# Optimization experiments

Measured on AMD Instinct MI355X. Metric: run time of the kernel, lower is better.

## Reference

```python
import jax, jax.numpy as jnp
import numpy as np


def gcn_conv(x, edge_index, edge_weight, W, b):
    """PyG-style GCNConv: add self-loops, symmetric normalization, sum aggregation."""
    N = x.shape[0]
    h = x @ W  # [N, out]
    src, dst = edge_index[0], edge_index[1]
    loop = jnp.arange(N, dtype=src.dtype)
    src2 = jnp.concatenate([src, loop])
    dst2 = jnp.concatenate([dst, loop])
    w2 = jnp.concatenate([edge_weight, jnp.ones((N,), dtype=edge_weight.dtype)])
    deg = jax.ops.segment_sum(w2, dst2, num_segments=N)  # [N]
    dinv = jnp.where(deg > 0, jax.lax.rsqrt(jnp.where(deg > 0, deg, 1.0)), 0.0)
    norm = dinv[src2] * w2 * dinv[dst2]  # [E+N]
    msg = h[src2] * norm[:, None]  # [E+N, out]
    out = jax.ops.segment_sum(msg, dst2, num_segments=N)  # [N, out]
    return out + b


def setup_inputs() -> dict:
    key = jax.random.key(0)
    ks = jax.random.split(key, 10)
    N, E, F = 100000, 3200000, 128
    x = jax.random.normal(ks[0], (N, F), dtype=jnp.float32)
    edge_index = jax.random.randint(ks[1], (2, E), 0, N, dtype=jnp.int64)
    edge_weight = jax.random.uniform(ks[2], (E,), dtype=jnp.float32)
    s1 = 1.0 / np.sqrt(F)
    W1 = jax.random.uniform(ks[3], (F, 32), jnp.float32, -s1, s1)
    b1 = jnp.zeros((32,), jnp.float32)
    s2 = 1.0 / np.sqrt(32)
    W2 = jax.random.uniform(ks[4], (32, 16), jnp.float32, -s2, s2)
    b2 = jnp.zeros((16,), jnp.float32)
    s3 = 1.0 / np.sqrt(16)
    Wout = jax.random.uniform(ks[5], (16, 3), jnp.float32, -s3, s3)
    bout = jax.random.uniform(ks[6], (3,), jnp.float32, -s3, s3)
    return {"x": x, "edge_index": edge_index, "edge_weight": edge_weight,
            "W1": W1, "b1": b1, "W2": W2, "b2": b2, "Wout": Wout, "bout": bout}


def reference(x, edge_index, edge_weight, W1, b1, W2, b2, Wout, bout):
    h = jax.nn.relu(gcn_conv(x, edge_index, edge_weight, W1, b1))
    h = jax.nn.relu(gcn_conv(h, edge_index, edge_weight, W2, b2))
    return h @ Wout + bout  # [N, 3]
```

## Files before the change

kernel.cpp:

```cpp
#include <hip/hip_runtime.h>


#define BLK 256

__global__ void deg_kernel(const int* __restrict__ dst,
                           const float* __restrict__ w,
                           float* __restrict__ deg, int E) {
    int e = blockIdx.x * blockDim.x + threadIdx.x;
    if (e < E) atomicAdd(&deg[dst[e]], w[e]);
}

__global__ void dinv_kernel(float* __restrict__ deg, int N) {
    int i = blockIdx.x * blockDim.x + threadIdx.x;
    if (i < N) deg[i] = rsqrtf(deg[i] + 1.0f);
}

__global__ void gemm1_kernel(const float* __restrict__ x,
                             const float* __restrict__ W1,
                             const float* __restrict__ dinv,
                             float* __restrict__ g1, int N) {
    __shared__ float sW[128 * 32];
    __shared__ float sx[8][128];
    for (int i = threadIdx.x; i < 128 * 32; i += BLK) sW[i] = W1[i];
    int node0 = blockIdx.x * 8;
    for (int i = threadIdx.x; i < 8 * 128; i += BLK) {
        int r = i >> 7, c = i & 127;
        int n = node0 + r;
        sx[r][c] = (n < N) ? x[(long long)n * 128 + c] : 0.f;
    }
    __syncthreads();
    int local = threadIdx.x >> 5;
    int j = threadIdx.x & 31;
    int n = node0 + local;
    if (n < N) {
        float acc = 0.f;
#pragma unroll 16
        for (int k = 0; k < 128; k++) acc += sx[local][k] * sW[k * 32 + j];
        g1[n * 32 + j] = acc * dinv[n];
    }
}

template <int F>
__global__ void edge_agg_kernel(const int* __restrict__ src,
                                const int* __restrict__ dst,
                                const float* __restrict__ w,
                                const float* __restrict__ g,
                                float* __restrict__ agg, int E) {
    unsigned idx = blockIdx.x * blockDim.x + threadIdx.x;
    unsigned total = (unsigned)E * F;
    if (idx >= total) return;
    unsigned e = idx / F;
    unsigned f = idx & (F - 1);
    int s = __ldg(&src[e]);
    int d = __ldg(&dst[e]);
    float we = __ldg(&w[e]);
    atomicAdd(&agg[(unsigned)d * F + f], we * g[(unsigned)s * F + f]);
}

__global__ void layer2_kernel(const float* __restrict__ agg1,
                              const float* __restrict__ g1,
                              const float* __restrict__ dinv,
                              const float* __restrict__ b1,
                              const float* __restrict__ W2,
                              float* __restrict__ g2, int N) {
    __shared__ float sW[32 * 16];
    __shared__ float sin_[16][32];
    for (int i = threadIdx.x; i < 32 * 16; i += BLK) sW[i] = W2[i];
    int node0 = blockIdx.x * 16;
    for (int i = threadIdx.x; i < 16 * 32; i += BLK) {
        int r = i >> 5, c = i & 31;
        int n = node0 + r;
        float v = 0.f;
        if (n < N) {
            float di = dinv[n];
            v = fmaxf(di * (agg1[n * 32 + c] + g1[n * 32 + c]) + b1[c], 0.f);
        }
        sin_[r][c] = v;
    }
    __syncthreads();
    int local = threadIdx.x >> 4;
    int j = threadIdx.x & 15;
    int n = node0 + local;
    if (n < N) {
        float acc = 0.f;
#pragma unroll
        for (int k = 0; k < 32; k++) acc += sin_[local][k] * sW[k * 16 + j];
        g2[n * 16 + j] = acc * dinv[n];
    }
}

__global__ void final_kernel(const float* __restrict__ agg2,
                             const float* __restrict__ g2,
                             const float* __restrict__ dinv,
                             const float* __restrict__ b2,
                             const float* __restrict__ Wout,
                             const float* __restrict__ bout,
                             float* __restrict__ out, int N) {
    int n = blockIdx.x * blockDim.x + threadIdx.x;
    if (n >= N) return;
    float di = dinv[n];
    float o0 = bout[0], o1 = bout[1], o2 = bout[2];
#pragma unroll
    for (int k = 0; k < 16; k++) {
        float v = fmaxf(di * (agg2[n * 16 + k] + g2[n * 16 + k]) + b2[k], 0.f);
        o0 += v * Wout[k * 3 + 0];
        o1 += v * Wout[k * 3 + 1];
        o2 += v * Wout[k * 3 + 2];
    }
    out[n * 3 + 0] = o0;
    out[n * 3 + 1] = o1;
    out[n * 3 + 2] = o2;
}

extern "C" void kernel_launch(void* const* d_in, const int* in_sizes, int n_in,
                              void* d_out, int out_size, void* d_ws, size_t ws_size,
                              hipStream_t stream) {
    const float* x   = (const float*)d_in[0];
    const int* ei    = (const int*)d_in[1];
    const float* ew  = (const float*)d_in[2];
    const float* W1  = (const float*)d_in[3];
    const float* b1  = (const float*)d_in[4];
    const float* W2  = (const float*)d_in[5];
    const float* b2  = (const float*)d_in[6];
    const float* Wout = (const float*)d_in[7];
    const float* bout = (const float*)d_in[8];
    float* out = (float*)d_out;

    const int N = in_sizes[0] / 128;
    const int E = in_sizes[2];
    const int* src = ei;
    const int* dst = ei + E;

    float* ws   = (float*)d_ws;
    float* deg  = ws;
    float* agg1 = ws + (size_t)N;
    float* agg2 = ws + (size_t)33 * N;
    float* g1   = ws + (size_t)49 * N;
    float* g2   = ws + (size_t)81 * N;

    hipMemsetAsync(ws, 0, (size_t)49 * N * sizeof(float), stream);

    deg_kernel<<<(E + BLK - 1) / BLK, BLK, 0, stream>>>(dst, ew, deg, E);
    dinv_kernel<<<(N + BLK - 1) / BLK, BLK, 0, stream>>>(deg, N);

    gemm1_kernel<<<(N + 7) / 8, BLK, 0, stream>>>(x, W1, deg, g1, N);

    {
        unsigned total = (unsigned)E * 32u;
        edge_agg_kernel<32><<<(total + BLK - 1) / BLK, BLK, 0, stream>>>(
            src, dst, ew, g1, agg1, E);
    }

    layer2_kernel<<<(N + 15) / 16, BLK, 0, stream>>>(agg1, g1, deg, b1, W2, g2, N);

    {
        unsigned total = (unsigned)E * 16u;
        edge_agg_kernel<16><<<(total + BLK - 1) / BLK, BLK, 0, stream>>>(
            src, dst, ew, g2, agg2, E);
    }

    final_kernel<<<(N + BLK - 1) / BLK, BLK, 0, stream>>>(
        agg2, g2, deg, b2, Wout, bout, out, N);
}
```

Baseline: 836.0 us.

## Build CSR by destination and replace atomic push aggregation with pull

Counts in-degrees, prefix-scans them into row pointers and scatters (src, weight) pairs into a destination-sorted CSR array on every call. Aggregation then becomes a per-node, per-feature pull loop with no float atomics, and bias plus ReLU are fused into that loop. This removes the per-feature atomic traffic of the old edge kernels. In exchange it adds the CSR construction cost (an extra atomic histogram and a scatter with atomics over all edges), and the pull loop is imbalanced across nodes of different degree.

```diff
diff --git a/kernel.cpp b/kernel.cpp
--- a/kernel.cpp
+++ b/kernel.cpp
@@ -3,17 +3,81 @@
 
 #define BLK 256
 
-__global__ void deg_kernel(const int* __restrict__ dst,
-                           const float* __restrict__ w,
-                           float* __restrict__ deg, int E) {
+
+__global__ void hist_kernel(const int* __restrict__ dst,
+                            const float* __restrict__ w,
+                            int* __restrict__ cnt,
+                            float* __restrict__ deg, int E) {
     int e = blockIdx.x * blockDim.x + threadIdx.x;
-    if (e < E) atomicAdd(&deg[dst[e]], w[e]);
+    if (e < E) {
+        int d = dst[e];
+        atomicAdd(&cnt[d], 1);
+        atomicAdd(&deg[d], w[e]);
+    }
 }
 
 __global__ void dinv_kernel(float* __restrict__ deg, int N) {
     int i = blockIdx.x * blockDim.x + threadIdx.x;
     if (i < N) deg[i] = rsqrtf(deg[i] + 1.0f);
 }
+
+__global__ void scan1_kernel(const int* __restrict__ cnt,
+                             int* __restrict__ rowptr,
+                             int* __restrict__ bsums, int N) {
+    __shared__ int tmp[BLK];
+    int i = blockIdx.x * BLK + threadIdx.x;
+    int v = (i < N) ? cnt[i] : 0;
+    tmp[threadIdx.x] = v;
+    __syncthreads();
+    for (int off = 1; off < BLK; off <<= 1) {
+        int t = (threadIdx.x >= off) ? tmp[threadIdx.x - off] : 0;
+        __syncthreads();
+        tmp[threadIdx.x] += t;
+        __syncthreads();
+    }
+    if (i < N) rowptr[i] = tmp[threadIdx.x] - v;
+    if (threadIdx.x == BLK - 1) bsums[blockIdx.x] = tmp[BLK - 1];
+}
+
+__global__ void scan2_kernel(int* __restrict__ bsums, int M) {
+    __shared__ int tmp[1024];
+    int v = (threadIdx.x < M) ? bsums[threadIdx.x] : 0;
+    tmp[threadIdx.x] = v;
+    __syncthreads();
+    for (int off = 1; off < 1024; off <<= 1) {
+        int t = (threadIdx.x >= off) ? tmp[threadIdx.x - off] : 0;
+        __syncthreads();
+        tmp[threadIdx.x] += t;
+        __syncthreads();
+    }
+    if (threadIdx.x < M) bsums[threadIdx.x] = tmp[threadIdx.x] - v;
+}
+
+__global__ void scan3_kernel(int* __restrict__ rowptr,
+                             int* __restrict__ cursor,
+                             const int* __restrict__ bsums, int N, int E) {
+    int i = blockIdx.x * BLK + threadIdx.x;
+    if (i < N) {
+        int r = rowptr[i] + bsums[blockIdx.x];
+        rowptr[i] = r;
+        cursor[i] = r;
+    }
+    if (i == 0) rowptr[N] = E;
+}
+
+__global__ void scatter_kernel(const int* __restrict__ src,
+                               const int* __restrict__ dst,
+                               const float* __restrict__ w,
+                               int* __restrict__ cursor,
+                               uint2* __restrict__ csr, int E) {
+    int e = blockIdx.x * blockDim.x + threadIdx.x;
+    if (e < E) {
+        int d = dst[e];
+        int pos = atomicAdd(&cursor[d], 1);
+        csr[pos] = make_uint2((unsigned)src[e], __float_as_uint(w[e]));
+    }
+}
+
 
 __global__ void gemm1_kernel(const float* __restrict__ x,
                              const float* __restrict__ W1,
@@ -40,29 +104,10 @@
     }
 }
 
-template <int F>
-__global__ void edge_agg_kernel(const int* __restrict__ src,
-                                const int* __restrict__ dst,
-                                const float* __restrict__ w,
-                                const float* __restrict__ g,
-                                float* __restrict__ agg, int E) {
-    unsigned idx = blockIdx.x * blockDim.x + threadIdx.x;
-    unsigned total = (unsigned)E * F;
-    if (idx >= total) return;
-    unsigned e = idx / F;
-    unsigned f = idx & (F - 1);
-    int s = __ldg(&src[e]);
-    int d = __ldg(&dst[e]);
-    float we = __ldg(&w[e]);
-    atomicAdd(&agg[(unsigned)d * F + f], we * g[(unsigned)s * F + f]);
-}
-
-__global__ void layer2_kernel(const float* __restrict__ agg1,
-                              const float* __restrict__ g1,
-                              const float* __restrict__ dinv,
-                              const float* __restrict__ b1,
-                              const float* __restrict__ W2,
-                              float* __restrict__ g2, int N) {
+__global__ void gemm2_kernel(const float* __restrict__ h1,
+                             const float* __restrict__ dinv,
+                             const float* __restrict__ W2,
+                             float* __restrict__ g2, int N) {
     __shared__ float sW[32 * 16];
     __shared__ float sin_[16][32];
     for (int i = threadIdx.x; i < 32 * 16; i += BLK) sW[i] = W2[i];
@@ -70,12 +115,7 @@
     for (int i = threadIdx.x; i < 16 * 32; i += BLK) {
         int r = i >> 5, c = i & 31;
         int n = node0 + r;
-        float v = 0.f;
-        if (n < N) {
-            float di = dinv[n];
-            v = fmaxf(di * (agg1[n * 32 + c] + g1[n * 32 + c]) + b1[c], 0.f);
-        }
-        sin_[r][c] = v;
+        sin_[r][c] = (n < N) ? h1[n * 32 + c] : 0.f;
     }
     __syncthreads();
     int local = threadIdx.x >> 4;
@@ -89,20 +129,36 @@
     }
 }
 
-__global__ void final_kernel(const float* __restrict__ agg2,
-                             const float* __restrict__ g2,
-                             const float* __restrict__ dinv,
-                             const float* __restrict__ b2,
+template <int F>
+__global__ void pull_kernel(const int* __restrict__ rowptr,
+                            const uint2* __restrict__ csr,
+                            const float* __restrict__ g,
+                            const float* __restrict__ dinv,
+                            const float* __restrict__ b,
+                            float* __restrict__ h, int N) {
+    unsigned idx = blockIdx.x * BLK + threadIdx.x;
+    unsigned n = idx / F;
+    unsigned f = idx & (F - 1);
+    if (n >= (unsigned)N) return;
+    int r0 = rowptr[n], r1 = rowptr[n + 1];
+    float acc = g[n * F + f];
+    for (int i = r0; i < r1; i++) {
+        uint2 e = csr[i];
+        acc += __uint_as_float(e.y) * g[(size_t)e.x * F + f];
+    }
+    h[n * F + f] = fmaxf(dinv[n] * acc + b[f], 0.f);
+}
+
+__global__ void final_kernel(const float* __restrict__ h2,
                              const float* __restrict__ Wout,
                              const float* __restrict__ bout,
                              float* __restrict__ out, int N) {
     int n = blockIdx.x * blockDim.x + threadIdx.x;
     if (n >= N) return;
-    float di = dinv[n];
     float o0 = bout[0], o1 = bout[1], o2 = bout[2];
 #pragma unroll
     for (int k = 0; k < 16; k++) {
-        float v = fmaxf(di * (agg2[n * 16 + k] + g2[n * 16 + k]) + b2[k], 0.f);
+        float v = h2[n * 16 + k];
         o0 += v * Wout[k * 3 + 0];
         o1 += v * Wout[k * 3 + 1];
         o2 += v * Wout[k * 3 + 2];
@@ -115,13 +171,13 @@
 extern "C" void kernel_launch(void* const* d_in, const int* in_sizes, int n_in,
                               void* d_out, int out_size, void* d_ws, size_t ws_size,
                               hipStream_t stream) {
-    const float* x   = (const float*)d_in[0];
-    const int* ei    = (const int*)d_in[1];
-    const float* ew  = (const float*)d_in[2];
-    const float* W1  = (const float*)d_in[3];
-    const float* b1  = (const float*)d_in[4];
-    const float* W2  = (const float*)d_in[5];
-    const float* b2  = (const float*)d_in[6];
+    const float* x    = (const float*)d_in[0];
+    const int* ei     = (const int*)d_in[1];
+    const float* ew   = (const float*)d_in[2];
+    const float* W1   = (const float*)d_in[3];
+    const float* b1   = (const float*)d_in[4];
+    const float* W2   = (const float*)d_in[5];
+    const float* b2   = (const float*)d_in[6];
     const float* Wout = (const float*)d_in[7];
     const float* bout = (const float*)d_in[8];
     float* out = (float*)d_out;
@@ -130,35 +186,41 @@
     const int E = in_sizes[2];
     const int* src = ei;
     const int* dst = ei + E;
+    const int NB = (N + BLK - 1) / BLK;
 
     float* ws   = (float*)d_ws;
     float* deg  = ws;
-    float* agg1 = ws + (size_t)N;
-    float* agg2 = ws + (size_t)33 * N;
-    float* g1   = ws + (size_t)49 * N;
-    float* g2   = ws + (size_t)81 * N;
-
-    hipMemsetAsync(ws, 0, (size_t)49 * N * sizeof(float), stream);
-
-    deg_kernel<<<(E + BLK - 1) / BLK, BLK, 0, stream>>>(dst, ew, deg, E);
-    dinv_kernel<<<(N + BLK - 1) / BLK, BLK, 0, stream>>>(deg, N);
+    int* cnt    = (int*)(ws + N);
+    int* rowptr = cnt + N;
+    int* cursor = rowptr + N + 1;
+    int* bsums  = cursor + N;
+    size_t off  = (size_t)4 * N + 1 + 1024;
+    off = (off + 1) & ~(size_t)1;
+    uint2* csr  = (uint2*)(ws + off);
+    float* g1   = (float*)(csr + E);
+    float* h1   = g1 + (size_t)32 * N;
+    float* g2   = h1 + (size_t)32 * N;
+    float* h2   = g1;
+
+    hipMemsetAsync(ws, 0, (size_t)2 * N * sizeof(float), stream);
+
+    hist_kernel<<<(E + BLK - 1) / BLK, BLK, 0, stream>>>(dst, ew, cnt, deg, E);
+    dinv_kernel<<<NB, BLK, 0, stream>>>(deg, N);
+
+    scan1_kernel<<<NB, BLK, 0, stream>>>(cnt, rowptr, bsums, N);
+    scan2_kernel<<<1, 1024, 0, stream>>>(bsums, NB);
+    scan3_kernel<<<NB, BLK, 0, stream>>>(rowptr, cursor, bsums, N, E);
+    scatter_kernel<<<(E + BLK - 1) / BLK, BLK, 0, stream>>>(src, dst, ew, cursor, csr, E);
 
     gemm1_kernel<<<(N + 7) / 8, BLK, 0, stream>>>(x, W1, deg, g1, N);
 
-    {
-        unsigned total = (unsigned)E * 32u;
-        edge_agg_kernel<32><<<(total + BLK - 1) / BLK, BLK, 0, stream>>>(
-            src, dst, ew, g1, agg1, E);
-    }
-
-    layer2_kernel<<<(N + 15) / 16, BLK, 0, stream>>>(agg1, g1, deg, b1, W2, g2, N);
-
-    {
-        unsigned total = (unsigned)E * 16u;
-        edge_agg_kernel<16><<<(total + BLK - 1) / BLK, BLK, 0, stream>>>(
-            src, dst, ew, g2, agg2, E);
-    }
-
-    final_kernel<<<(N + BLK - 1) / BLK, BLK, 0, stream>>>(
-        agg2, g2, deg, b2, Wout, bout, out, N);
-}
+    pull_kernel<32><<<((unsigned)N * 32 + BLK - 1) / BLK, BLK, 0, stream>>>(
+        rowptr, csr, g1, deg, b1, h1, N);
+
+    gemm2_kernel<<<(N + 15) / 16, BLK, 0, stream>>>(h1, deg, W2, g2, N);
+
+    pull_kernel<16><<<((unsigned)N * 16 + BLK - 1) / BLK, BLK, 0, stream>>>(
+        rowptr, csr, g2, deg, b2, h2, N);
+
+    final_kernel<<<NB, BLK, 0, stream>>>(h2, Wout, bout, out, N);
+}
```

After: 955.2 us. +14.3%, slower.

## Bucket edges by destination and aggregate with shared-memory atomics

Applied to the files above, without the earlier changes.

Replaces per-feature global atomic scatter with a counting sort of edges into 256-node destination buckets, storing packed (src, local dst, weight) records. Each bucket block then accumulates messages in a shared-memory tile and applies normalization, self-loop, bias and ReLU in the epilogue, and degree is computed the same way. This removes global float atomics and the workspace memset, at the cost of a sort pass and only one block per 256 nodes, which limits parallelism.

```diff
diff --git a/kernel.cpp b/kernel.cpp
--- a/kernel.cpp
+++ b/kernel.cpp
@@ -1,24 +1,98 @@
 #include <hip/hip_runtime.h>
 
 
+#define G 256
 #define BLK 256
 
-__global__ void deg_kernel(const int* __restrict__ dst,
-                           const float* __restrict__ w,
-                           float* __restrict__ deg, int E) {
-    int e = blockIdx.x * blockDim.x + threadIdx.x;
-    if (e < E) atomicAdd(&deg[dst[e]], w[e]);
-}
-
-__global__ void dinv_kernel(float* __restrict__ deg, int N) {
-    int i = blockIdx.x * blockDim.x + threadIdx.x;
-    if (i < N) deg[i] = rsqrtf(deg[i] + 1.0f);
-}
-
-__global__ void gemm1_kernel(const float* __restrict__ x,
-                             const float* __restrict__ W1,
-                             const float* __restrict__ dinv,
-                             float* __restrict__ g1, int N) {
+
+__global__ __launch_bounds__(256) void hist_kernel(
+    const int* __restrict__ dst, int* __restrict__ blockHist, int E, int B) {
+    __shared__ int hist[512];
+    for (int i = threadIdx.x; i < B; i += 256) hist[i] = 0;
+    __syncthreads();
+    int per = (E + G - 1) / G;
+    int e0 = blockIdx.x * per, e1 = min(e0 + per, E);
+    for (int e = e0 + threadIdx.x; e < e1; e += 256)
+        atomicAdd(&hist[((unsigned)dst[e]) >> 8], 1);
+    __syncthreads();
+    for (int i = threadIdx.x; i < B; i += 256)
+        blockHist[i * G + blockIdx.x] = hist[i];
+}
+
+__global__ __launch_bounds__(256) void scan_cols_kernel(
+    int* __restrict__ blockHist, int* __restrict__ bucketTotal) {
+    __shared__ int tmp[256];
+    int b = blockIdx.x;
+    int v = blockHist[b * G + threadIdx.x];
+    tmp[threadIdx.x] = v;
+    __syncthreads();
+    for (int off = 1; off < 256; off <<= 1) {
+        int t = (threadIdx.x >= off) ? tmp[threadIdx.x - off] : 0;
+        __syncthreads();
+        tmp[threadIdx.x] += t;
+        __syncthreads();
+    }
+    blockHist[b * G + threadIdx.x] = tmp[threadIdx.x] - v;
+    if (threadIdx.x == 255) bucketTotal[b] = tmp[255];
+}
+
+__global__ void base_scan_kernel(const int* __restrict__ bucketTotal,
+                                 int* __restrict__ bucketBase, int B, int E) {
+    __shared__ int tmp[512];
+    int v = (threadIdx.x < B) ? bucketTotal[threadIdx.x] : 0;
+    tmp[threadIdx.x] = v;
+    __syncthreads();
+    for (int off = 1; off < 512; off <<= 1) {
+        int t = (threadIdx.x >= off) ? tmp[threadIdx.x - off] : 0;
+        __syncthreads();
+        tmp[threadIdx.x] += t;
+        __syncthreads();
+    }
+    if (threadIdx.x < B) bucketBase[threadIdx.x] = tmp[threadIdx.x] - v;
+    if (threadIdx.x == 0) bucketBase[B] = E;
+}
+
+__global__ __launch_bounds__(256) void scatter_kernel(
+    const int* __restrict__ src, const int* __restrict__ dst,
+    const float* __restrict__ w, const int* __restrict__ blockHist,
+    const int* __restrict__ bucketBase, uint2* __restrict__ recs,
+    int E, int B) {
+    __shared__ int cursor[512];
+    for (int i = threadIdx.x; i < B; i += 256)
+        cursor[i] = bucketBase[i] + blockHist[i * G + blockIdx.x];
+    __syncthreads();
+    int per = (E + G - 1) / G;
+    int e0 = blockIdx.x * per, e1 = min(e0 + per, E);
+    for (int e = e0 + threadIdx.x; e < e1; e += 256) {
+        int d = dst[e];
+        int b = ((unsigned)d) >> 8;
+        int pos = atomicAdd(&cursor[b], 1);
+        recs[pos] = make_uint2((unsigned)src[e] | ((unsigned)(d & 255) << 20),
+                               __float_as_uint(w[e]));
+    }
+}
+
+__global__ __launch_bounds__(256) void degdinv_kernel(
+    const int* __restrict__ bucketBase, const uint2* __restrict__ recs,
+    float* __restrict__ dinv, int N) {
+    __shared__ float deg[256];
+    deg[threadIdx.x] = 0.f;
+    __syncthreads();
+    int b = blockIdx.x;
+    int r0 = bucketBase[b], r1 = bucketBase[b + 1];
+    for (int i = r0 + threadIdx.x; i < r1; i += 256) {
+        uint2 rec = recs[i];
+        atomicAdd(&deg[rec.x >> 20], __uint_as_float(rec.y));
+    }
+    __syncthreads();
+    int n = b * 256 + threadIdx.x;
+    if (n < N) dinv[n] = rsqrtf(deg[threadIdx.x] + 1.f);
+}
+
+
+__global__ __launch_bounds__(256) void gemm1_kernel(
+    const float* __restrict__ x, const float* __restrict__ W1,
+    float* __restrict__ u1, int N) {
     __shared__ float sW[128 * 32];
     __shared__ float sx[8][128];
     for (int i = threadIdx.x; i < 128 * 32; i += BLK) sW[i] = W1[i];
@@ -26,7 +100,7 @@
     for (int i = threadIdx.x; i < 8 * 128; i += BLK) {
         int r = i >> 7, c = i & 127;
         int n = node0 + r;
-        sx[r][c] = (n < N) ? x[(long long)n * 128 + c] : 0.f;
+        sx[r][c] = (n < N) ? x[(size_t)n * 128 + c] : 0.f;
     }
     __syncthreads();
     int local = threadIdx.x >> 5;
@@ -36,33 +110,13 @@
         float acc = 0.f;
 #pragma unroll 16
         for (int k = 0; k < 128; k++) acc += sx[local][k] * sW[k * 32 + j];
-        g1[n * 32 + j] = acc * dinv[n];
-    }
-}
-
-template <int F>
-__global__ void edge_agg_kernel(const int* __restrict__ src,
-                                const int* __restrict__ dst,
-                                const float* __restrict__ w,
-                                const float* __restrict__ g,
-                                float* __restrict__ agg, int E) {
-    unsigned idx = blockIdx.x * blockDim.x + threadIdx.x;
-    unsigned total = (unsigned)E * F;
-    if (idx >= total) return;
-    unsigned e = idx / F;
-    unsigned f = idx & (F - 1);
-    int s = __ldg(&src[e]);
-    int d = __ldg(&dst[e]);
-    float we = __ldg(&w[e]);
-    atomicAdd(&agg[(unsigned)d * F + f], we * g[(unsigned)s * F + f]);
-}
-
-__global__ void layer2_kernel(const float* __restrict__ agg1,
-                              const float* __restrict__ g1,
-                              const float* __restrict__ dinv,
-                              const float* __restrict__ b1,
-                              const float* __restrict__ W2,
-                              float* __restrict__ g2, int N) {
+        u1[(size_t)n * 32 + j] = acc;
+    }
+}
+
+__global__ __launch_bounds__(256) void gemm2_kernel(
+    const float* __restrict__ h1, const float* __restrict__ W2,
+    float* __restrict__ u2, int N) {
     __shared__ float sW[32 * 16];
     __shared__ float sin_[16][32];
     for (int i = threadIdx.x; i < 32 * 16; i += BLK) sW[i] = W2[i];
@@ -70,12 +124,7 @@
     for (int i = threadIdx.x; i < 16 * 32; i += BLK) {
         int r = i >> 5, c = i & 31;
         int n = node0 + r;
-        float v = 0.f;
-        if (n < N) {
-            float di = dinv[n];
-            v = fmaxf(di * (agg1[n * 32 + c] + g1[n * 32 + c]) + b1[c], 0.f);
-        }
-        sin_[r][c] = v;
+        sin_[r][c] = (n < N) ? h1[(size_t)n * 32 + c] : 0.f;
     }
     __syncthreads();
     int local = threadIdx.x >> 4;
@@ -85,24 +134,52 @@
         float acc = 0.f;
 #pragma unroll
         for (int k = 0; k < 32; k++) acc += sin_[local][k] * sW[k * 16 + j];
-        g2[n * 16 + j] = acc * dinv[n];
-    }
-}
-
-__global__ void final_kernel(const float* __restrict__ agg2,
-                             const float* __restrict__ g2,
-                             const float* __restrict__ dinv,
-                             const float* __restrict__ b2,
-                             const float* __restrict__ Wout,
-                             const float* __restrict__ bout,
-                             float* __restrict__ out, int N) {
+        u2[(size_t)n * 16 + j] = acc;
+    }
+}
+
+template <int F>
+__global__ __launch_bounds__(256) void agg_kernel(
+    const int* __restrict__ bucketBase, const uint2* __restrict__ recs,
+    const float* __restrict__ u, const float* __restrict__ dinv,
+    const float* __restrict__ bias, float* __restrict__ h, int N) {
+    const int FS = F + 1;
+    __shared__ float tile[256 * FS];
+    for (int i = threadIdx.x; i < 256 * FS; i += 256) tile[i] = 0.f;
+    __syncthreads();
+    int b = blockIdx.x;
+    int r0 = bucketBase[b], r1 = bucketBase[b + 1];
+    const int EPB = 256 / F;
+    int f = threadIdx.x & (F - 1);
+    for (int i = r0 + (threadIdx.x / F); i < r1; i += EPB) {
+        uint2 rec = recs[i];
+        unsigned s  = rec.x & 0xFFFFFu;
+        unsigned dl = rec.x >> 20;
+        float wdi = __uint_as_float(rec.y) * dinv[s];
+        atomicAdd(&tile[dl * FS + f], wdi * u[(size_t)s * F + f]);
+    }
+    __syncthreads();
+    int node0 = b * 256;
+    for (int k = threadIdx.x; k < 256 * F; k += 256) {
+        int loc = k / F, ff = k & (F - 1);
+        int n = node0 + loc;
+        if (n < N) {
+            float di = dinv[n];
+            float v = di * tile[loc * FS + ff] + di * di * u[(size_t)n * F + ff] + bias[ff];
+            h[(size_t)n * F + ff] = fmaxf(v, 0.f);
+        }
+    }
+}
+
+__global__ __launch_bounds__(256) void final_kernel(
+    const float* __restrict__ h2, const float* __restrict__ Wout,
+    const float* __restrict__ bout, float* __restrict__ out, int N) {
     int n = blockIdx.x * blockDim.x + threadIdx.x;
     if (n >= N) return;
-    float di = dinv[n];
     float o0 = bout[0], o1 = bout[1], o2 = bout[2];
 #pragma unroll
     for (int k = 0; k < 16; k++) {
-        float v = fmaxf(di * (agg2[n * 16 + k] + g2[n * 16 + k]) + b2[k], 0.f);
+        float v = h2[(size_t)n * 16 + k];
         o0 += v * Wout[k * 3 + 0];
         o1 += v * Wout[k * 3 + 1];
         o2 += v * Wout[k * 3 + 2];
@@ -115,13 +192,13 @@
 extern "C" void kernel_launch(void* const* d_in, const int* in_sizes, int n_in,
                               void* d_out, int out_size, void* d_ws, size_t ws_size,
                               hipStream_t stream) {
-    const float* x   = (const float*)d_in[0];
-    const int* ei    = (const int*)d_in[1];
-    const float* ew  = (const float*)d_in[2];
-    const float* W1  = (const float*)d_in[3];
-    const float* b1  = (const float*)d_in[4];
-    const float* W2  = (const float*)d_in[5];
-    const float* b2  = (const float*)d_in[6];
+    const float* x    = (const float*)d_in[0];
+    const int* ei     = (const int*)d_in[1];
+    const float* ew   = (const float*)d_in[2];
+    const float* W1   = (const float*)d_in[3];
+    const float* b1   = (const float*)d_in[4];
+    const float* W2   = (const float*)d_in[5];
+    const float* b2   = (const float*)d_in[6];
     const float* Wout = (const float*)d_in[7];
     const float* bout = (const float*)d_in[8];
     float* out = (float*)d_out;
@@ -130,35 +207,28 @@
     const int E = in_sizes[2];
     const int* src = ei;
     const int* dst = ei + E;
-
-    float* ws   = (float*)d_ws;
-    float* deg  = ws;
-    float* agg1 = ws + (size_t)N;
-    float* agg2 = ws + (size_t)33 * N;
-    float* g1   = ws + (size_t)49 * N;
-    float* g2   = ws + (size_t)81 * N;
-
-    hipMemsetAsync(ws, 0, (size_t)49 * N * sizeof(float), stream);
-
-    deg_kernel<<<(E + BLK - 1) / BLK, BLK, 0, stream>>>(dst, ew, deg, E);
-    dinv_kernel<<<(N + BLK - 1) / BLK, BLK, 0, stream>>>(deg, N);
-
-    gemm1_kernel<<<(N + 7) / 8, BLK, 0, stream>>>(x, W1, deg, g1, N);
-
-    {
-        unsigned total = (unsigned)E * 32u;
-        edge_agg_kernel<32><<<(total + BLK - 1) / BLK, BLK, 0, stream>>>(
-            src, dst, ew, g1, agg1, E);
-    }
-
-    layer2_kernel<<<(N + 15) / 16, BLK, 0, stream>>>(agg1, g1, deg, b1, W2, g2, N);
-
-    {
-        unsigned total = (unsigned)E * 16u;
-        edge_agg_kernel<16><<<(total + BLK - 1) / BLK, BLK, 0, stream>>>(
-            src, dst, ew, g2, agg2, E);
-    }
-
-    final_kernel<<<(N + BLK - 1) / BLK, BLK, 0, stream>>>(
-        agg2, g2, deg, b2, Wout, bout, out, N);
-}
+    const int B = (N + 255) >> 8;
+
+    float* ws = (float*)d_ws;
+    uint2* recs = (uint2*)ws;
+    float* u1   = ws + (size_t)2 * E;
+    float* h1   = u1 + (size_t)32 * N;
+    float* u2   = h1 + (size_t)32 * N;
+    float* dinv = u2 + (size_t)16 * N;
+    int* blockHist   = (int*)(dinv + N);
+    int* bucketTotal = blockHist + (size_t)B * G;
+    int* bucketBase  = bucketTotal + B;
+    float* h2 = u1;
+
+    hist_kernel<<<G, 256, 0, stream>>>(dst, blockHist, E, B);
+    scan_cols_kernel<<<B, 256, 0, stream>>>(blockHist, bucketTotal);
+    base_scan_kernel<<<1, 512, 0, stream>>>(bucketTotal, bucketBase, B, E);
+    scatter_kernel<<<G, 256, 0, stream>>>(src, dst, ew, blockHist, bucketBase, recs, E, B);
+    degdinv_kernel<<<B, 256, 0, stream>>>(bucketBase, recs, dinv, N);
+
+    gemm1_kernel<<<(N + 7) / 8, 256, 0, stream>>>(x, W1, u1, N);
+    agg_kernel<32><<<B, 256, 0, stream>>>(bucketBase, recs, u1, dinv, b1, h1, N);
+    gemm2_kernel<<<(N + 15) / 16, 256, 0, stream>>>(h1, W2, u2, N);
+    agg_kernel<16><<<B, 256, 0, stream>>>(bucketBase, recs, u2, dinv, b2, h2, N);
+    final_kernel<<<(N + 255) / 256, 256, 0, stream>>>(h2, Wout, bout, out, N);
+}
```

New measurement: 1.319 ms. +57.8%, slower.
